# Kernel optimization log

Measured on AMD Instinct MI355X. Metric: run time of the kernel, lower is better.

## Reference

```python
import jax, jax.numpy as jnp
import numpy as np

HEADS = 16
DIM_HEAD = 64
SCALE = DIM_HEAD ** -0.5


def setup_inputs() -> dict:
    key = jax.random.key(0)
    ks = jax.random.split(key, 5)
    dim = 1024
    inner = HEADS * DIM_HEAD  # 1024
    x = jax.random.normal(ks[0], (2, 2048, dim), dtype=jnp.float32)
    # Linear weights stored as [in, out] so y = x @ W
    s = dim ** -0.5
    Wq = jax.random.normal(ks[1], (dim, inner), dtype=jnp.float32) * s
    Wk = jax.random.normal(ks[2], (dim, inner), dtype=jnp.float32) * s
    Wv = jax.random.normal(ks[3], (dim, inner), dtype=jnp.float32) * s
    Wo = jax.random.normal(ks[4], (inner, dim), dtype=jnp.float32) * s
    bo = jnp.zeros((dim,), dtype=jnp.float32)
    return {"x": x, "Wq": Wq, "Wk": Wk, "Wv": Wv, "Wo": Wo, "bo": bo}


def reference(x, Wq, Wk, Wv, Wo, bo):
    b, n, _ = x.shape
    def split_heads(t):  # [b, n, h*d] -> [b, h, n, d]
        return t.reshape(b, n, HEADS, DIM_HEAD).transpose(0, 2, 1, 3)
    q = split_heads(x @ Wq)
    k = split_heads(x @ Wk)
    v = split_heads(x @ Wv)
    sim = jnp.einsum('bhid,bhjd->bhij', q, k) * SCALE  # [b, h, n, n]
    attn = jax.nn.softmax(sim, axis=-1)
    out = jnp.einsum('bhij,bhjd->bhid', attn, v)  # [b, h, n, d]
    out = out.transpose(0, 2, 1, 3).reshape(b, n, HEADS * DIM_HEAD)
    return out @ Wo + bo
```

## Files before the change

kernel.cpp:

```cpp
#include <hip/hip_runtime.h>
#include <hip/hip_fp16.h>

typedef _Float16 f16;
typedef __attribute__((ext_vector_type(8))) _Float16 half8;
typedef __attribute__((ext_vector_type(2))) __fp16 fp16x2_native;
typedef __attribute__((ext_vector_type(4))) float floatx4;
typedef __attribute__((ext_vector_type(16))) float f32x16;
typedef __attribute__((ext_vector_type(4))) unsigned uint4v;
typedef __attribute__((ext_vector_type(2))) unsigned uint2v;

static constexpr int DIM = 1024;
static constexpr int SEQ = 2048;
static constexpr int DH = 64;
static constexpr int MTOT = 4096;

__device__ __forceinline__ float fexp2(float x) {
#if __has_builtin(__builtin_amdgcn_exp2f)
  return __builtin_amdgcn_exp2f(x);
#else
  return exp2f(x);
#endif
}

__device__ __forceinline__ unsigned pkrtz(float a, float b) {
  fp16x2_native h = __builtin_amdgcn_cvt_pkrtz(a, b);
  return __builtin_bit_cast(unsigned, h);
}

__device__ __forceinline__ void pl32swap(unsigned& a, unsigned& b) {
#if __has_builtin(__builtin_amdgcn_permlane32_swap)
  uint2v r = __builtin_amdgcn_permlane32_swap(a, b, false, false);
  a = r.x;
  b = r.y;
#else
  asm volatile("v_permlane32_swap_b32 %0, %1" : "+v"(a), "+v"(b));
#endif
}

__device__ __forceinline__ void gll16(const f16* g, f16* l) {
  auto gp = (__attribute__((address_space(1))) unsigned*)(uintptr_t)(const void*)g;
  auto lp = (__attribute__((address_space(3))) unsigned*)(uintptr_t)(void*)l;
  __builtin_amdgcn_global_load_lds(gp, lp, 16, 0, 0);
}

__global__ __launch_bounds__(256) void k_transpose(
    const float* __restrict__ Wq, const float* __restrict__ Wk,
    const float* __restrict__ Wv, const float* __restrict__ Wo,
    f16* __restrict__ wt)
{
  __shared__ float tile[32][33];
  const int z = blockIdx.z;
  const float* W = (z == 0) ? Wq : (z == 1) ? Wk : (z == 2) ? Wv : Wo;
  f16* out = wt + (size_t)z * DIM * DIM;
  const int tx = threadIdx.x, ty = threadIdx.y;
  const int x0 = blockIdx.x * 32, y0 = blockIdx.y * 32;
#pragma unroll
  for (int i = 0; i < 4; ++i)
    tile[ty + i * 8][tx] = W[(size_t)(y0 + ty + i * 8) * DIM + (x0 + tx)];
  __syncthreads();
#pragma unroll
  for (int i = 0; i < 4; ++i)
    out[(size_t)(x0 + ty + i * 8) * DIM + (y0 + tx)] = (f16)tile[tx][ty + i * 8];
}

__global__ __launch_bounds__(256) void k_xcast(
    const float* __restrict__ in, f16* __restrict__ out)
{
  const int i = blockIdx.x * 256 + threadIdx.x;
  const float4* p = (const float4*)in;
  float4 a = p[2 * i], b = p[2 * i + 1];
  half8 h = {(f16)a.x, (f16)a.y, (f16)a.z, (f16)a.w,
             (f16)b.x, (f16)b.y, (f16)b.z, (f16)b.w};
  *(half8*)(out + (size_t)i * 8) = h;
}

__global__ __launch_bounds__(256) void k_vtrans(
    const f16* __restrict__ vh, f16* __restrict__ vt)
{
  __shared__ f16 T[64][72];
  const int tid = threadIdx.x;
  const int nt = blockIdx.x, bh = blockIdx.y;
  const int b = bh >> 4, h = bh & 15;
  const int n0 = nt * 64;
  const f16* src = vh + (size_t)b * SEQ * DIM + (size_t)h * DH;
#pragma unroll
  for (int i = 0; i < 2; ++i) {
    const int n = (tid >> 3) + i * 32;
    const int cc = tid & 7;
    half8 v = *(const half8*)(src + (size_t)(n0 + n) * DIM + cc * 8);
#pragma unroll
    for (int j = 0; j < 8; ++j) T[cc * 8 + j][n] = v[j];
  }
  __syncthreads();
  f16* dst = vt + (size_t)bh * DH * SEQ;
#pragma unroll
  for (int i = 0; i < 2; ++i) {
    const int d = (tid >> 3) + i * 32;
    const int cc = tid & 7;
    half8 w = *(const half8*)&T[d][cc * 8];
    *(half8*)(dst + (size_t)d * SEQ + n0 + cc * 8) = w;
  }
}

template <bool OUT_F32>
__global__ __launch_bounds__(256) void k_gemm2(
    const f16* __restrict__ A, const f16* __restrict__ BT,
    void* __restrict__ Cptr, const float* __restrict__ bias,
    int M, int N, int K, size_t bt_zstride, size_t c_zstride)
{
  __shared__ f16 SB[2][8192];

  const int tid = threadIdx.x;
  const int lane = tid & 63;
  const int wid = tid >> 6;
  const int wr = (wid >> 1) * 64, wc = (wid & 1) * 64;
  const int li = lane & 15, lg = lane >> 4;

  const f16* BTz = BT + (size_t)blockIdx.z * bt_zstride;
  const int row0 = blockIdx.x * 128, col0 = blockIdx.y * 128;

  const int c0 = tid;
  const int c1 = 256 + tid;
  const f16* a0 = A + (size_t)(row0 + (c0 >> 2)) * K + (c0 & 3) * 8;
  const f16* a1 = A + (size_t)(row0 + (c1 >> 2)) * K + (c1 & 3) * 8;
  const f16* b0 = BTz + (size_t)(col0 + (c0 >> 2)) * K + (c0 & 3) * 8;
  const f16* b1 = BTz + (size_t)(col0 + (c1 >> 2)) * K + (c1 & 3) * 8;
  const int da0 = wid * 512, da1 = 2048 + wid * 512;

  const floatx4 zero4 = {0.f, 0.f, 0.f, 0.f};
  floatx4 acc[4][4];
#pragma unroll
  for (int m = 0; m < 4; ++m)
#pragma unroll
    for (int n = 0; n < 4; ++n) acc[m][n] = zero4;

  auto issue = [&](int buf) {
    gll16(a0, &SB[buf][da0]);
    gll16(a1, &SB[buf][da1]);
    gll16(b0, &SB[buf][4096 + da0]);
    gll16(b1, &SB[buf][4096 + da1]);
    a0 += 32; a1 += 32; b0 += 32; b1 += 32;
  };

  const int nstep = K >> 5;
  issue(0);

  auto step = [&](int buf, int t) {
    asm volatile("s_waitcnt vmcnt(0)" ::: "memory");
    __builtin_amdgcn_s_barrier();
    asm volatile("" ::: "memory");
    if (t + 1 < nstep) issue(buf ^ 1);
    const f16* As = &SB[buf][0];
    const f16* Bs = &SB[buf][4096];
    half8 af[4], bf[4];
#pragma unroll
    for (int m = 0; m < 4; ++m)
      af[m] = *(const half8*)&As[(wr + m * 16 + li) * 32 + lg * 8];
#pragma unroll
    for (int n = 0; n < 4; ++n)
      bf[n] = *(const half8*)&Bs[(wc + n * 16 + li) * 32 + lg * 8];
#pragma unroll
    for (int m = 0; m < 4; ++m)
#pragma unroll
      for (int n = 0; n < 4; ++n)
        acc[m][n] = __builtin_amdgcn_mfma_f32_16x16x32_f16(af[m], bf[n], acc[m][n], 0, 0, 0);
  };

  for (int t2 = 0; t2 < nstep; t2 += 2) {
    step(0, t2);
    step(1, t2 + 1);
  }

#pragma unroll
  for (int m = 0; m < 4; ++m)
#pragma unroll
    for (int n = 0; n < 4; ++n)
#pragma unroll
      for (int r = 0; r < 4; ++r) {
        const int row = row0 + wr + m * 16 + lg * 4 + r;
        const int col = col0 + wc + n * 16 + li;
        if constexpr (OUT_F32) {
          float* C = (float*)Cptr + (size_t)blockIdx.z * c_zstride;
          C[(size_t)row * N + col] = acc[m][n][r] + bias[col];
        } else {
          f16* C = (f16*)Cptr + (size_t)blockIdx.z * c_zstride;
          C[(size_t)row * N + col] = (f16)acc[m][n][r];
        }
      }
}

__global__ __launch_bounds__(512) void k_attn4(
    const f16* __restrict__ qh, const f16* __restrict__ kh,
    const f16* __restrict__ vt, f16* __restrict__ oh)
{
  __shared__ f16 KV[2][16384];
  __shared__ float bc[8][32];
  __shared__ float Lm[4][32], Ll[4][32], W0[4][32], W1[4][32];

  const int tid = threadIdx.x;
  const int lane = tid & 63;
  const int wid = tid >> 6;
  const int g = wid >> 2;
  const int sub = wid & 3;
  const int col = lane & 31;
  const int hi = lane >> 5;

  const int id = blockIdx.x;
  const int xcd = id & 7;
  const int j = id >> 3;
  const int bh = xcd * 4 + (j >> 4);
  const int qi = j & 15;
  const int b = bh >> 4, h = bh & 15;

  const int q0 = qi * 128 + sub * 32;
  const size_t xbase = (size_t)b * SEQ * DIM + (size_t)h * DH;
  const size_t vtbase = (size_t)bh * DH * SEQ;

  const float SC = 0.125f * 1.44269504089f;
  const float RTRAW = 8.0f / SC;

  const int lc = tid & 511;
  const int srow = lc >> 3;
  const int sw = ((lc & 7) ^ (srow & 7)) * 8;
  const f16* ks0 = kh + xbase + (size_t)srow * DIM + sw;
  const f16* ks1 = kh + xbase + (size_t)(1024 + srow) * DIM + sw;
  const f16* vs0 = vt + vtbase + (size_t)srow * SEQ + sw;
  const f16* vs1 = vt + vtbase + (size_t)srow * SEQ + 1024 + sw;

  auto issue = [&](int buf) {
    f16* B = &KV[buf][wid * 512];
    gll16(ks0, B);
    gll16(vs0, B + 4096);
    gll16(ks1, B + 8192);
    gll16(vs1, B + 12288);
    ks0 += 64 * DIM; ks1 += 64 * DIM; vs0 += 64; vs1 += 64;
  };

  half8 qb[4];
  {
    const f16* qrow = qh + xbase + (size_t)(q0 + col) * DIM;
#pragma unroll
    for (int s = 0; s < 4; ++s) qb[s] = *(const half8*)(qrow + s * 16 + hi * 8);
  }

  f32x16 o0 = {0, 0, 0, 0, 0, 0, 0, 0, 0, 0, 0, 0, 0, 0, 0, 0};
  f32x16 o1 = {0, 0, 0, 0, 0, 0, 0, 0, 0, 0, 0, 0, 0, 0, 0, 0};
  float m = -1e30f, lsum = 0.f;

  issue(0);

  auto tile = [&](int buf, int t) {
    asm volatile("s_waitcnt vmcnt(0)" ::: "memory");
    __builtin_amdgcn_s_barrier();
    asm volatile("" ::: "memory");
    if (t < 15) issue(buf ^ 1);
    const f16* Ks = &KV[buf][g * 8192];
    const f16* Vs = Ks + 4096;

#pragma unroll
    for (int kvs = 0; kvs < 2; ++kvs) {
      const int krow = kvs * 32 + col;
      f32x16 sacc = {0, 0, 0, 0, 0, 0, 0, 0, 0, 0, 0, 0, 0, 0, 0, 0};
      __builtin_amdgcn_s_setprio(1);
#pragma unroll
      for (int s = 0; s < 4; ++s) {
        const int cc = (2 * s + hi) ^ (krow & 7);
        half8 ka = *(const half8*)&Ks[krow * 64 + cc * 8];
        sacc = __builtin_amdgcn_mfma_f32_32x32x16_f16(ka, qb[s], sacc, 0, 0, 0);
      }
      __builtin_amdgcn_s_setprio(0);

      float x0 = fmaxf(fmaxf(sacc[0], sacc[1]), fmaxf(sacc[2], sacc[3]));
      float x1 = fmaxf(fmaxf(sacc[4], sacc[5]), fmaxf(sacc[6], sacc[7]));
      float x2 = fmaxf(fmaxf(sacc[8], sacc[9]), fmaxf(sacc[10], sacc[11]));
      float x3 = fmaxf(fmaxf(sacc[12], sacc[13]), fmaxf(sacc[14], sacc[15]));
      float smax = fmaxf(fmaxf(x0, x1), fmaxf(x2, x3));
      smax = fmaxf(smax, __shfl_xor(smax, 32));

      if (!__all(smax <= m + RTRAW)) {
        const float mn = fmaxf(m, smax);
        const float alpha = fexp2((m - mn) * SC);
        m = mn;
        lsum *= alpha;
        if (hi == 0) bc[wid][col] = alpha;
#pragma unroll
        for (int r = 0; r < 16; ++r) {
          const float a2 = bc[wid][(r & 3) + 8 * (r >> 2) + 4 * hi];
          o0[r] *= a2;
          o1[r] *= a2;
        }
      }

      const float mc = m * SC;
      float pw[16];
#pragma unroll
      for (int r = 0; r < 16; ++r) pw[r] = fexp2(fmaf(sacc[r], SC, -mc));
      float s0 = (pw[0] + pw[1]) + (pw[2] + pw[3]);
      float s1 = (pw[4] + pw[5]) + (pw[6] + pw[7]);
      float s2 = (pw[8] + pw[9]) + (pw[10] + pw[11]);
      float s3 = (pw[12] + pw[13]) + (pw[14] + pw[15]);
      float rs = (s0 + s1) + (s2 + s3);
      rs += __shfl_xor(rs, 32);
      lsum += rs;

      __builtin_amdgcn_s_setprio(1);
#pragma unroll
      for (int s2i = 0; s2i < 2; ++s2i) {
        const int rb = s2i * 8;
        unsigned X0 = pkrtz(pw[rb + 0], pw[rb + 1]);
        unsigned X1 = pkrtz(pw[rb + 2], pw[rb + 3]);
        unsigned Y0 = pkrtz(pw[rb + 4], pw[rb + 5]);
        unsigned Y1 = pkrtz(pw[rb + 6], pw[rb + 7]);
        pl32swap(X0, Y0);
        pl32swap(X1, Y1);
        const half8 paf = __builtin_bit_cast(half8, (uint4v){X0, X1, Y0, Y1});
        const int kc = kvs * 4 + s2i * 2 + hi;
#pragma unroll
        for (int dt = 0; dt < 2; ++dt) {
          const int vrow = dt * 32 + col;
          const int cc = kc ^ (vrow & 7);
          half8 vb = *(const half8*)&Vs[vrow * 64 + cc * 8];
          if (dt == 0)
            o0 = __builtin_amdgcn_mfma_f32_32x32x16_f16(paf, vb, o0, 0, 0, 0);
          else
            o1 = __builtin_amdgcn_mfma_f32_32x32x16_f16(paf, vb, o1, 0, 0, 0);
        }
      }
      __builtin_amdgcn_s_setprio(0);
    }
  };

  for (int t2 = 0; t2 < 16; t2 += 2) {
    tile(0, t2);
    tile(1, t2 + 1);
  }

  const float inv = 1.0f / lsum;
  if (hi == 0) bc[wid][col] = inv;
  if (g == 1) {
    if (hi == 0) { Lm[sub][col] = m; Ll[sub][col] = lsum; }
    f16* po = &KV[0][0] + sub * 2048;
#pragma unroll
    for (int r = 0; r < 16; ++r) {
      const int qr = (r & 3) + 8 * (r >> 2) + 4 * hi;
      const float iv = bc[wid][qr];
      po[qr * 64 + col] = (f16)(o0[r] * iv);
      po[qr * 64 + 32 + col] = (f16)(o1[r] * iv);
    }
  }
  __syncthreads();
  if (g == 0) {
    const float m1 = Lm[sub][col], l1 = Ll[sub][col];
    const float M = fmaxf(m, m1);
    const float e0 = fexp2((m - M) * SC);
    const float a0 = lsum * e0;
    const float a1 = l1 * fexp2((m1 - M) * SC);
    const float rden = 1.0f / (a0 + a1);
    const float c0 = e0 * rden;
    const float w1 = a1 * rden;
    if (hi == 0) { W0[sub][col] = c0; W1[sub][col] = w1; }
    const f16* po = &KV[0][0] + sub * 2048;
#pragma unroll
    for (int r = 0; r < 16; ++r) {
      const int qr = (r & 3) + 8 * (r >> 2) + 4 * hi;
      const float c0r = W0[sub][qr], w1r = W1[sub][qr];
      f16* orow = oh + xbase + (size_t)(q0 + qr) * DIM;
      orow[col] = (f16)(c0r * o0[r] + w1r * (float)po[qr * 64 + col]);
      orow[32 + col] = (f16)(c0r * o1[r] + w1r * (float)po[qr * 64 + 32 + col]);
    }
  }
}

extern "C" void kernel_launch(void* const* d_in, const int* in_sizes, int n_in,
                              void* d_out, int out_size, void* d_ws, size_t ws_size,
                              hipStream_t stream)
{
  const float* x  = (const float*)d_in[0];
  const float* Wq = (const float*)d_in[1];
  const float* Wk = (const float*)d_in[2];
  const float* Wv = (const float*)d_in[3];
  const float* Wo = (const float*)d_in[4];
  const float* bo = (const float*)d_in[5];

  char* ws = (char*)d_ws;
  f16* wt   = (f16*)ws;
  f16* qkvh = (f16*)(ws + (size_t)8 * 1024 * 1024);
  f16* ohp  = (f16*)(ws + (size_t)32 * 1024 * 1024);
  f16* vtb  = (f16*)(ws + (size_t)40 * 1024 * 1024);
  f16* xh   = ohp;

  k_transpose<<<dim3(32, 32, 4), dim3(32, 8), 0, stream>>>(Wq, Wk, Wv, Wo, wt);

  k_xcast<<<2048, 256, 0, stream>>>(x, xh);

  k_gemm2<false><<<dim3(32, 8, 3), 256, 0, stream>>>(
      xh, wt, qkvh, nullptr, MTOT, DIM, DIM,
      (size_t)DIM * DIM, (size_t)MTOT * DIM);

  k_vtrans<<<dim3(32, 32), 256, 0, stream>>>(
      qkvh + (size_t)2 * MTOT * DIM, vtb);

  k_attn4<<<512, 512, 0, stream>>>(
      qkvh, qkvh + (size_t)MTOT * DIM, vtb, ohp);

  k_gemm2<true><<<dim3(32, 8, 1), 256, 0, stream>>>(
      ohp, wt + (size_t)3 * DIM * DIM, d_out, bo, MTOT, DIM, DIM, 0, 0);
}
```

Measured before the change: 120.7 us.

## Fuse prep kernels, add smaller-tile output GEMM, defer row-sum shuffle

```diff
diff --git a/kernel.cpp b/kernel.cpp
--- a/kernel.cpp
+++ b/kernel.cpp
@@ -43,16 +43,28 @@
   __builtin_amdgcn_global_load_lds(gp, lp, 16, 0, 0);
 }
 
-__global__ __launch_bounds__(256) void k_transpose(
+__global__ __launch_bounds__(256) void k_prep(
     const float* __restrict__ Wq, const float* __restrict__ Wk,
     const float* __restrict__ Wv, const float* __restrict__ Wo,
-    f16* __restrict__ wt)
-{
+    const float* __restrict__ x, f16* __restrict__ wt, f16* __restrict__ xh)
+{
+  const int z = blockIdx.z;
+  const int tx = threadIdx.x, ty = threadIdx.y;
+  if (z == 4) {
+    const int i = (blockIdx.y * 32 + blockIdx.x) * 256 + ty * 32 + tx;
+    const float4* p = (const float4*)x + (size_t)i * 4;
+    float4 v0 = p[0], v1 = p[1], v2 = p[2], v3 = p[3];
+    half8 h0 = {(f16)v0.x, (f16)v0.y, (f16)v0.z, (f16)v0.w,
+                (f16)v1.x, (f16)v1.y, (f16)v1.z, (f16)v1.w};
+    half8 h1 = {(f16)v2.x, (f16)v2.y, (f16)v2.z, (f16)v2.w,
+                (f16)v3.x, (f16)v3.y, (f16)v3.z, (f16)v3.w};
+    *(half8*)(xh + (size_t)i * 16) = h0;
+    *(half8*)(xh + (size_t)i * 16 + 8) = h1;
+    return;
+  }
   __shared__ float tile[32][33];
-  const int z = blockIdx.z;
   const float* W = (z == 0) ? Wq : (z == 1) ? Wk : (z == 2) ? Wv : Wo;
   f16* out = wt + (size_t)z * DIM * DIM;
-  const int tx = threadIdx.x, ty = threadIdx.y;
   const int x0 = blockIdx.x * 32, y0 = blockIdx.y * 32;
 #pragma unroll
   for (int i = 0; i < 4; ++i)
@@ -61,17 +73,6 @@
 #pragma unroll
   for (int i = 0; i < 4; ++i)
     out[(size_t)(x0 + ty + i * 8) * DIM + (y0 + tx)] = (f16)tile[tx][ty + i * 8];
-}
-
-__global__ __launch_bounds__(256) void k_xcast(
-    const float* __restrict__ in, f16* __restrict__ out)
-{
-  const int i = blockIdx.x * 256 + threadIdx.x;
-  const float4* p = (const float4*)in;
-  float4 a = p[2 * i], b = p[2 * i + 1];
-  half8 h = {(f16)a.x, (f16)a.y, (f16)a.z, (f16)a.w,
-             (f16)b.x, (f16)b.y, (f16)b.z, (f16)b.w};
-  *(half8*)(out + (size_t)i * 8) = h;
 }
 
 __global__ __launch_bounds__(256) void k_vtrans(
@@ -189,7 +190,81 @@
       }
 }
 
-__global__ __launch_bounds__(512) void k_attn4(
+__global__ __launch_bounds__(256) void k_gemm3(
+    const f16* __restrict__ A, const f16* __restrict__ BT,
+    float* __restrict__ C, const float* __restrict__ bias)
+{
+  __shared__ f16 SB[2][6144];
+
+  const int tid = threadIdx.x;
+  const int lane = tid & 63;
+  const int wid = tid >> 6;
+  const int wr = (wid >> 1) * 64, wc = (wid & 1) * 32;
+  const int li = lane & 15, lg = lane >> 4;
+
+  const int row0 = blockIdx.x * 128, col0 = blockIdx.y * 64;
+
+  const int c0 = tid, c1 = tid + 256;
+  const f16* a0 = A + (size_t)(row0 + (c0 >> 2)) * DIM + (c0 & 3) * 8;
+  const f16* a1 = A + (size_t)(row0 + (c1 >> 2)) * DIM + (c1 & 3) * 8;
+  const f16* b0 = BT + (size_t)(col0 + (tid >> 2)) * DIM + (tid & 3) * 8;
+
+  const floatx4 zero4 = {0.f, 0.f, 0.f, 0.f};
+  floatx4 acc[4][2];
+#pragma unroll
+  for (int m = 0; m < 4; ++m)
+#pragma unroll
+    for (int n = 0; n < 2; ++n) acc[m][n] = zero4;
+
+  auto issue = [&](int buf) {
+    f16* B = &SB[buf][0];
+    gll16(a0, B + tid * 8);
+    gll16(a1, B + 2048 + tid * 8);
+    gll16(b0, B + 4096 + tid * 8);
+    a0 += 32; a1 += 32; b0 += 32;
+  };
+
+  issue(0);
+
+  auto step = [&](int buf, int t) {
+    asm volatile("s_waitcnt vmcnt(0)" ::: "memory");
+    __builtin_amdgcn_s_barrier();
+    asm volatile("" ::: "memory");
+    if (t + 1 < 32) issue(buf ^ 1);
+    const f16* As = &SB[buf][0];
+    const f16* Bs = &SB[buf][4096];
+    half8 af[4], bf[2];
+#pragma unroll
+    for (int m = 0; m < 4; ++m)
+      af[m] = *(const half8*)&As[(wr + m * 16 + li) * 32 + lg * 8];
+#pragma unroll
+    for (int n = 0; n < 2; ++n)
+      bf[n] = *(const half8*)&Bs[(wc + n * 16 + li) * 32 + lg * 8];
+#pragma unroll
+    for (int m = 0; m < 4; ++m)
+#pragma unroll
+      for (int n = 0; n < 2; ++n)
+        acc[m][n] = __builtin_amdgcn_mfma_f32_16x16x32_f16(af[m], bf[n], acc[m][n], 0, 0, 0);
+  };
+
+  for (int t2 = 0; t2 < 32; t2 += 2) {
+    step(0, t2);
+    step(1, t2 + 1);
+  }
+
+#pragma unroll
+  for (int m = 0; m < 4; ++m)
+#pragma unroll
+    for (int n = 0; n < 2; ++n)
+#pragma unroll
+      for (int r = 0; r < 4; ++r) {
+        const int row = row0 + wr + m * 16 + lg * 4 + r;
+        const int col = col0 + wc + n * 16 + li;
+        C[(size_t)row * DIM + col] = acc[m][n][r] + bias[col];
+      }
+}
+
+__global__ __launch_bounds__(512) void k_attn8(
     const f16* __restrict__ qh, const f16* __restrict__ kh,
     const f16* __restrict__ vt, f16* __restrict__ oh)
 {
@@ -299,9 +374,7 @@
       float s1 = (pw[4] + pw[5]) + (pw[6] + pw[7]);
       float s2 = (pw[8] + pw[9]) + (pw[10] + pw[11]);
       float s3 = (pw[12] + pw[13]) + (pw[14] + pw[15]);
-      float rs = (s0 + s1) + (s2 + s3);
-      rs += __shfl_xor(rs, 32);
-      lsum += rs;
+      lsum += (s0 + s1) + (s2 + s3);
 
       __builtin_amdgcn_s_setprio(1);
 #pragma unroll
@@ -335,10 +408,11 @@
     tile(1, t2 + 1);
   }
 
-  const float inv = 1.0f / lsum;
-  if (hi == 0) bc[wid][col] = inv;
+  lsum += __shfl_xor(lsum, 32);
+
   if (g == 1) {
-    if (hi == 0) { Lm[sub][col] = m; Ll[sub][col] = lsum; }
+    const float inv = 1.0f / lsum;
+    if (hi == 0) { Lm[sub][col] = m; Ll[sub][col] = lsum; bc[wid][col] = inv; }
     f16* po = &KV[0][0] + sub * 2048;
 #pragma unroll
     for (int r = 0; r < 16; ++r) {
@@ -389,9 +463,7 @@
   f16* vtb  = (f16*)(ws + (size_t)40 * 1024 * 1024);
   f16* xh   = ohp;
 
-  k_transpose<<<dim3(32, 32, 4), dim3(32, 8), 0, stream>>>(Wq, Wk, Wv, Wo, wt);
-
-  k_xcast<<<2048, 256, 0, stream>>>(x, xh);
+  k_prep<<<dim3(32, 32, 5), dim3(32, 8), 0, stream>>>(Wq, Wk, Wv, Wo, x, wt, xh);
 
   k_gemm2<false><<<dim3(32, 8, 3), 256, 0, stream>>>(
       xh, wt, qkvh, nullptr, MTOT, DIM, DIM,
@@ -400,9 +472,9 @@
   k_vtrans<<<dim3(32, 32), 256, 0, stream>>>(
       qkvh + (size_t)2 * MTOT * DIM, vtb);
 
-  k_attn4<<<512, 512, 0, stream>>>(
+  k_attn8<<<512, 512, 0, stream>>>(
       qkvh, qkvh + (size_t)MTOT * DIM, vtb, ohp);
 
-  k_gemm2<true><<<dim3(32, 8, 1), 256, 0, stream>>>(
-      ohp, wt + (size_t)3 * DIM * DIM, d_out, bo, MTOT, DIM, DIM, 0, 0);
-}
+  k_gemm3<<<dim3(32, 16), 256, 0, stream>>>(
+      ohp, wt + (size_t)3 * DIM * DIM, (float*)d_out, bo);
+}
```

Result: faster. 116.5 us (-3.5%).
